# Performance work log

Hardware: AMD Instinct MI355X
Metric: run time of the kernel (lower is better)

## Reference

```python
import jax, jax.numpy as jnp
import numpy as np

FIELD = 32
DIM = 64
LAYER_SIZE = (128, 128)


def setup_inputs() -> dict:
    key = jax.random.key(0)
    ks = jax.random.split(key, 5)
    B = 4096
    x = jax.random.normal(ks[0], (B, FIELD, DIM), dtype=jnp.float32)
    # conv1d kernel-size-1 weights, stored as [out_channels, in_channels]
    field_nums = [FIELD]
    params = {}
    for i, size in enumerate(LAYER_SIZE):
        in_ch = field_nums[-1] * field_nums[0]
        fan = 1.0 / np.sqrt(in_ch)
        params[f"w{i}"] = jax.random.uniform(ks[1 + 2 * i % 4], (size, in_ch), minval=-fan, maxval=fan, dtype=jnp.float32)
        params[f"b{i}"] = jax.random.uniform(ks[2 + 2 * i % 4], (size,), minval=-fan, maxval=fan, dtype=jnp.float32)
        field_nums.append(size // 2)
    return {"cin_inputs": x, "w0": params["w0"], "b0": params["b0"], "w1": params["w1"], "b1": params["b1"]}


def _cin(x, weights, biases):
    # x: [B, F, D]
    B, F, D = x.shape
    hidden = x
    finals = []
    n_layers = len(weights)
    for i, (w, b) in enumerate(zip(weights, biases)):
        size = w.shape[0]
        # outer product over field dims: [B, H, F, D] -> reshape to [B, H*F, D]
        z = jnp.einsum('bhd,bfd->bhfd', hidden, x).reshape(B, hidden.shape[1] * F, D)
        # 1x1 conv over channel dim == per-position matmul
        y = jnp.einsum('bcd,oc->bod', z, w) + b[None, :, None]
        y = jax.nn.relu(y)
        if i != n_layers - 1:
            hidden, direct = y[:, : size // 2, :], y[:, size // 2 :, :]
        else:
            direct = y
        finals.append(direct)
    return jnp.concatenate(finals, axis=1).sum(-1)  # [B, out_dim]


def reference(cin_inputs, w0, b0, w1, b1):
    return _cin(cin_inputs, [w0, w1], [b0, b1])
```

## Files before the change

### kernel.cpp

```cpp
#include <hip/hip_runtime.h>
#include <hip/hip_fp16.h>


typedef __attribute__((ext_vector_type(8))) _Float16 f16x8;
typedef __attribute__((ext_vector_type(4))) float f32x4;
typedef __attribute__((ext_vector_type(4))) unsigned short us4;
typedef unsigned short ushortT;

__global__ void cin_pack_w(const float* __restrict__ w0,
                           const float* __restrict__ w1,
                           ushortT* __restrict__ wp) {
    int gidx = blockIdx.x * 256 + threadIdx.x;
    if (gidx >= 49152) return;
    const float* src;
    ushortT* dst;
    if (gidx < 16384) {
        int kk = gidx >> 9, rem = gidx & 511;
        int n = rem >> 6, lp = rem & 63;
        int o = n * 16 + (lp & 15);
        int c = kk * 32 + ((lp >> 4) << 3);
        src = w0 + o * 1024 + c;
        dst = wp + gidx * 8;
    } else {
        int g1 = gidx - 16384;
        int kk = g1 >> 9, rem = g1 & 511;
        int n = rem >> 6, lp = rem & 63;
        int o = n * 16 + (lp & 15);
        int c = kk * 32 + ((lp >> 4) << 3);
        src = w1 + o * 2048 + c;
        dst = wp + 131072 + g1 * 8;
    }
    ushortT tmp[8];
#pragma unroll
    for (int j = 0; j < 8; ++j) {
        __half h = __float2half(src[j]);
        tmp[j] = __builtin_bit_cast(ushortT, h);
    }
    *reinterpret_cast<f16x8*>(dst) = *reinterpret_cast<const f16x8*>(tmp);
}

__global__ __launch_bounds__(256, 2) void cin_mfma_kernel(
    const float* __restrict__ x,
    const float* __restrict__ b0,
    const float* __restrict__ b1,
    const ushortT* __restrict__ wp,
    float* __restrict__ out)
{
    const int tid = threadIdx.x;
    const int l   = tid & 63;
    const int w   = tid >> 6;
    const int b   = blockIdx.x * 4 + w;
    const int r16 = l & 15;
    const int g   = l >> 4;

    __shared__ ushortT Xh[4][2048];
    __shared__ ushortT Hsm[4][64 * 66];
    __shared__ __align__(16) ushortT Wb[2][4096];

    ushortT* Xw = Xh[w];
    ushortT* Hw = Hsm[w];

    const float* xb = x + (size_t)b * 2048;
#pragma unroll
    for (int i = 0; i < 8; ++i) {
        float4 v = reinterpret_cast<const float4*>(xb)[i * 64 + l];
        int flat = (i * 64 + l) * 4;
        us4 h;
        h[0] = __builtin_bit_cast(ushortT, __float2half(v.x));
        h[1] = __builtin_bit_cast(ushortT, __float2half(v.y));
        h[2] = __builtin_bit_cast(ushortT, __float2half(v.z));
        h[3] = __builtin_bit_cast(ushortT, __float2half(v.w));
        *reinterpret_cast<us4*>(&Xw[flat]) = h;
    }

#pragma unroll
    for (int c = 0; c < 2; ++c) {
        const char* src = (const char*)wp + (size_t)c * 8192 +
                          (size_t)(w * 2) * 1024 + (size_t)l * 16;
        __builtin_amdgcn_global_load_lds((const unsigned int*)src,
                                         (unsigned int*)&Wb[c][(w * 2) * 512], 16, 0, 0);
        __builtin_amdgcn_global_load_lds((const unsigned int*)(src + 1024),
                                         (unsigned int*)&Wb[c][(w * 2 + 1) * 512], 16, 0, 0);
    }
    __syncthreads();

    __half2 tf16[4][4];
#pragma unroll
    for (int mt = 0; mt < 4; ++mt)
#pragma unroll
        for (int p = 0; p < 4; ++p) {
            unsigned lo = Xw[(g * 8 + 2 * p) * 64 + mt * 16 + r16];
            unsigned hi = Xw[(g * 8 + 2 * p + 1) * 64 + mt * 16 + r16];
            tf16[mt][p] = __builtin_bit_cast(__half2, lo | (hi << 16));
        }

    __half2 th[4];
#pragma unroll
    for (int mt = 0; mt < 4; ++mt) {
        unsigned u = Xw[mt * 16 + r16];
        th[mt] = __builtin_bit_cast(__half2, (u << 16) | u);
    }
    f16x8 Bf[8];
#pragma unroll
    for (int n = 0; n < 8; ++n)
        Bf[n] = *reinterpret_cast<const f16x8*>(&Wb[0][n * 512 + l * 8]);

    __syncthreads();

    f32x4 acc[4][8];
#pragma unroll
    for (int mt = 0; mt < 4; ++mt)
#pragma unroll
        for (int n = 0; n < 8; ++n) acc[mt][n] = (f32x4){0.f, 0.f, 0.f, 0.f};

#pragma unroll 1
    for (int k = 0; k < 96; ++k) {
        const int cur = k & 1;

        if (k + 2 < 96) {
            const char* src = (const char*)wp + (size_t)(k + 2) * 8192 +
                              (size_t)(w * 2) * 1024 + (size_t)l * 16;
            __builtin_amdgcn_global_load_lds((const unsigned int*)src,
                (unsigned int*)&Wb[cur][(w * 2) * 512], 16, 0, 0);
            __builtin_amdgcn_global_load_lds((const unsigned int*)(src + 1024),
                (unsigned int*)&Wb[cur][(w * 2 + 1) * 512], 16, 0, 0);
        }

        const bool pf_th = (k < 95) && (k != 31);
        const ushortT* WbN = Wb[(k < 95) ? (cur ^ 1) : cur];
        const ushortT* thp = (k + 1 < 32) ? (Xw + (k + 1) * 64)
                                          : (Hw + (k - 31) * 66);

        union AfU { __half2 h2[4]; f16x8 v; };
        AfU Af[4];
#pragma unroll
        for (int mt = 0; mt < 4; ++mt)
#pragma unroll
            for (int p = 0; p < 4; ++p)
                Af[mt].h2[p] = __hmul2(tf16[mt][p], th[mt]);

        if (pf_th) {
#pragma unroll
            for (int mt = 0; mt < 4; ++mt) {
                unsigned u = thp[mt * 16 + r16];
                th[mt] = __builtin_bit_cast(__half2, (u << 16) | u);
            }
        }

#pragma unroll
        for (int n = 0; n < 8; ++n) {
#pragma unroll
            for (int mt = 0; mt < 4; ++mt)
                acc[mt][n] = __builtin_amdgcn_mfma_f32_16x16x32_f16(
                    Af[mt].v, Bf[n], acc[mt][n], 0, 0, 0);
            Bf[n] = *reinterpret_cast<const f16x8*>(&WbN[n * 512 + l * 8]);
        }

        __syncthreads();

        if (k == 31) {
#pragma unroll
            for (int n = 0; n < 4; ++n) {
                float bn = b0[n * 16 + r16];
#pragma unroll
                for (int mt = 0; mt < 4; ++mt)
#pragma unroll
                    for (int r = 0; r < 4; ++r) {
                        float y = fmaxf(acc[mt][n][r] + bn, 0.f);
                        int d = mt * 16 + g * 4 + r;
                        int o = n * 16 + r16;
                        __half hy = __float2half(y);
                        Hw[o * 66 + d] = __builtin_bit_cast(ushortT, hy);
                    }
            }
#pragma unroll
            for (int n = 4; n < 8; ++n) {
                float bn = b0[n * 16 + r16];
                float s = 0.f;
#pragma unroll
                for (int mt = 0; mt < 4; ++mt)
#pragma unroll
                    for (int r = 0; r < 4; ++r)
                        s += fmaxf(acc[mt][n][r] + bn, 0.f);
                s += __shfl_xor(s, 16);
                s += __shfl_xor(s, 32);
                if (l < 16) out[(size_t)b * 192 + (n - 4) * 16 + l] = s;
            }
#pragma unroll
            for (int mt = 0; mt < 4; ++mt)
#pragma unroll
                for (int n = 0; n < 8; ++n) acc[mt][n] = (f32x4){0.f, 0.f, 0.f, 0.f};
#pragma unroll
            for (int mt = 0; mt < 4; ++mt) {
                unsigned u = Hw[mt * 16 + r16];
                th[mt] = __builtin_bit_cast(__half2, (u << 16) | u);
            }
        }
    }

#pragma unroll
    for (int n = 0; n < 8; ++n) {
        float bn = b1[n * 16 + r16];
        float s = 0.f;
#pragma unroll
        for (int mt = 0; mt < 4; ++mt)
#pragma unroll
            for (int r = 0; r < 4; ++r)
                s += fmaxf(acc[mt][n][r] + bn, 0.f);
        s += __shfl_xor(s, 16);
        s += __shfl_xor(s, 32);
        if (l < 16) out[(size_t)b * 192 + 64 + n * 16 + l] = s;
    }
}

__global__ __launch_bounds__(256, 4) void cin_fp32_kernel(
    const float* __restrict__ x, const float* __restrict__ w0,
    const float* __restrict__ b0, const float* __restrict__ w1,
    const float* __restrict__ b1, float* __restrict__ out)
{
    const int b = blockIdx.x;
    const int tid = threadIdx.x;
    const int d = tid & 63;
    const int wave = tid >> 6;

    __shared__ float Xs[32][64];
    __shared__ float Hsf[64][64];

    const float* xb = x + (size_t)b * 2048;
    float treg[32];
#pragma unroll
    for (int f = 0; f < 32; ++f) treg[f] = xb[f * 64 + d];
    if (wave == 0) {
#pragma unroll
        for (int f = 0; f < 32; ++f) Xs[f][d] = treg[f];
    }
    __syncthreads();
    const int o_base = __builtin_amdgcn_readfirstlane(wave * 32);

    for (int oi = 0; oi < 32; ++oi) {
        const int o = o_base + oi;
        const float* wrow = w0 + (size_t)o * 1024;
        float acc = b0[o];
        for (int h = 0; h < 32; ++h) {
            const float* wv = wrow + h * 32;
            const float th = Xs[h][d];
            float s0 = 0.f, s1 = 0.f, s2 = 0.f, s3 = 0.f;
#pragma unroll
            for (int f = 0; f < 32; f += 4) {
                s0 = fmaf(wv[f + 0], treg[f + 0], s0);
                s1 = fmaf(wv[f + 1], treg[f + 1], s1);
                s2 = fmaf(wv[f + 2], treg[f + 2], s2);
                s3 = fmaf(wv[f + 3], treg[f + 3], s3);
            }
            acc = fmaf((s0 + s1) + (s2 + s3), th, acc);
        }
        float y = fmaxf(acc, 0.f);
        if (o < 64) {
            Hsf[o][d] = y;
        } else {
#pragma unroll
            for (int off = 32; off > 0; off >>= 1) y += __shfl_xor(y, off, 64);
            if (d == 0) out[(size_t)b * 192 + (o - 64)] = y;
        }
    }
    __syncthreads();

    for (int oi = 0; oi < 32; ++oi) {
        const int o = o_base + oi;
        const float* wrow = w1 + (size_t)o * 2048;
        float acc = b1[o];
        for (int h = 0; h < 64; ++h) {
            const float* wv = wrow + h * 32;
            const float th = Hsf[h][d];
            float s0 = 0.f, s1 = 0.f, s2 = 0.f, s3 = 0.f;
#pragma unroll
            for (int f = 0; f < 32; f += 4) {
                s0 = fmaf(wv[f + 0], treg[f + 0], s0);
                s1 = fmaf(wv[f + 1], treg[f + 1], s1);
                s2 = fmaf(wv[f + 2], treg[f + 2], s2);
                s3 = fmaf(wv[f + 3], treg[f + 3], s3);
            }
            acc = fmaf((s0 + s1) + (s2 + s3), th, acc);
        }
        float y = fmaxf(acc, 0.f);
#pragma unroll
        for (int off = 32; off > 0; off >>= 1) y += __shfl_xor(y, off, 64);
        if (d == 0) out[(size_t)b * 192 + 64 + o] = y;
    }
}

extern "C" void kernel_launch(void* const* d_in, const int* in_sizes, int n_in,
                              void* d_out, int out_size, void* d_ws, size_t ws_size,
                              hipStream_t stream) {
    const float* x  = (const float*)d_in[0];
    const float* w0 = (const float*)d_in[1];
    const float* b0 = (const float*)d_in[2];
    const float* w1 = (const float*)d_in[3];
    const float* b1 = (const float*)d_in[4];
    float* out = (float*)d_out;

    if (ws_size >= 786432) {
        ushortT* wp = (ushortT*)d_ws;
        cin_pack_w<<<192, 256, 0, stream>>>(w0, w1, wp);
        cin_mfma_kernel<<<1024, 256, 0, stream>>>(x, b0, b1, wp, out);
    } else {
        cin_fp32_kernel<<<4096, 256, 0, stream>>>(x, w0, b0, w1, b1, out);
    }
}
```

Before: 169.1 us.

## Process two K-steps per iteration with larger double-buffered weight tiles

The K loop is restructured so each iteration handles two 32-channel steps. It streams a 16 KB weight chunk per stage into a double buffer, which halves the number of block barriers and async-load issue points. The hidden-layer tile now reuses the per-wave X region, unpadded, and is written with vectorized stores, so shared memory shrinks slightly. MFMA bursts are wrapped in s_setprio to favour matrix issue. In exchange, th values are reloaded from LDS each step, and register pressure rises from holding two sets of B fragments.

```diff
diff --git a/kernel.cpp b/kernel.cpp
--- a/kernel.cpp
+++ b/kernel.cpp
@@ -53,12 +53,10 @@
     const int r16 = l & 15;
     const int g   = l >> 4;
 
-    __shared__ ushortT Xh[4][2048];
-    __shared__ ushortT Hsm[4][64 * 66];
-    __shared__ __align__(16) ushortT Wb[2][4096];
-
-    ushortT* Xw = Xh[w];
-    ushortT* Hw = Hsm[w];
+    __shared__ ushortT U[4][4096];
+    __shared__ __align__(16) ushortT Wb[2][8192];
+
+    ushortT* Xw = U[w];
 
     const float* xb = x + (size_t)b * 2048;
 #pragma unroll
@@ -74,13 +72,11 @@
     }
 
 #pragma unroll
-    for (int c = 0; c < 2; ++c) {
-        const char* src = (const char*)wp + (size_t)c * 8192 +
-                          (size_t)(w * 2) * 1024 + (size_t)l * 16;
+    for (int j = 0; j < 4; ++j) {
+        const int seg = w * 4 + j;
+        const char* src = (const char*)wp + (size_t)seg * 1024 + (size_t)l * 16;
         __builtin_amdgcn_global_load_lds((const unsigned int*)src,
-                                         (unsigned int*)&Wb[c][(w * 2) * 512], 16, 0, 0);
-        __builtin_amdgcn_global_load_lds((const unsigned int*)(src + 1024),
-                                         (unsigned int*)&Wb[c][(w * 2 + 1) * 512], 16, 0, 0);
+                                         (unsigned int*)&Wb[0][seg * 512], 16, 0, 0);
     }
     __syncthreads();
 
@@ -94,84 +90,102 @@
             tf16[mt][p] = __builtin_bit_cast(__half2, lo | (hi << 16));
         }
 
-    __half2 th[4];
-#pragma unroll
-    for (int mt = 0; mt < 4; ++mt) {
-        unsigned u = Xw[mt * 16 + r16];
-        th[mt] = __builtin_bit_cast(__half2, (u << 16) | u);
-    }
-    f16x8 Bf[8];
-#pragma unroll
-    for (int n = 0; n < 8; ++n)
-        Bf[n] = *reinterpret_cast<const f16x8*>(&Wb[0][n * 512 + l * 8]);
-
-    __syncthreads();
-
     f32x4 acc[4][8];
 #pragma unroll
     for (int mt = 0; mt < 4; ++mt)
 #pragma unroll
         for (int n = 0; n < 8; ++n) acc[mt][n] = (f32x4){0.f, 0.f, 0.f, 0.f};
 
+    union AfU { __half2 h2[4]; f16x8 v; };
+
 #pragma unroll 1
-    for (int k = 0; k < 96; ++k) {
-        const int cur = k & 1;
-
-        if (k + 2 < 96) {
-            const char* src = (const char*)wp + (size_t)(k + 2) * 8192 +
-                              (size_t)(w * 2) * 1024 + (size_t)l * 16;
-            __builtin_amdgcn_global_load_lds((const unsigned int*)src,
-                (unsigned int*)&Wb[cur][(w * 2) * 512], 16, 0, 0);
-            __builtin_amdgcn_global_load_lds((const unsigned int*)(src + 1024),
-                (unsigned int*)&Wb[cur][(w * 2 + 1) * 512], 16, 0, 0);
-        }
-
-        const bool pf_th = (k < 95) && (k != 31);
-        const ushortT* WbN = Wb[(k < 95) ? (cur ^ 1) : cur];
-        const ushortT* thp = (k + 1 < 32) ? (Xw + (k + 1) * 64)
-                                          : (Hw + (k - 31) * 66);
-
-        union AfU { __half2 h2[4]; f16x8 v; };
+    for (int p = 0; p < 48; ++p) {
+        const int ps = p & 1;
+        const int k0 = 2 * p;
+
+        if (p + 1 < 48) {
+#pragma unroll
+            for (int j = 0; j < 4; ++j) {
+                const int seg = w * 4 + j;
+                const char* src = (const char*)wp + (size_t)(p + 1) * 16384 +
+                                  (size_t)seg * 1024 + (size_t)l * 16;
+                __builtin_amdgcn_global_load_lds((const unsigned int*)src,
+                    (unsigned int*)&Wb[ps ^ 1][seg * 512], 16, 0, 0);
+            }
+        }
+
+        const ushortT* th0p = Xw + (size_t)((k0 < 32) ? k0 : (k0 - 32)) * 64;
+        __half2 th[4];
+#pragma unroll
+        for (int mt = 0; mt < 4; ++mt) {
+            unsigned u = th0p[mt * 16 + r16];
+            th[mt] = __builtin_bit_cast(__half2, (u << 16) | u);
+        }
+
+        f16x8 Bf[8];
+#pragma unroll
+        for (int n = 0; n < 8; ++n)
+            Bf[n] = *reinterpret_cast<const f16x8*>(&Wb[ps][n * 512 + l * 8]);
+
         AfU Af[4];
 #pragma unroll
         for (int mt = 0; mt < 4; ++mt)
 #pragma unroll
-            for (int p = 0; p < 4; ++p)
-                Af[mt].h2[p] = __hmul2(tf16[mt][p], th[mt]);
-
-        if (pf_th) {
-#pragma unroll
-            for (int mt = 0; mt < 4; ++mt) {
-                unsigned u = thp[mt * 16 + r16];
-                th[mt] = __builtin_bit_cast(__half2, (u << 16) | u);
-            }
-        }
-
+            for (int q = 0; q < 4; ++q)
+                Af[mt].h2[q] = __hmul2(tf16[mt][q], th[mt]);
+
+        const int k1 = k0 + 1;
+        const ushortT* th1p = Xw + (size_t)((k1 < 32) ? k1 : (k1 - 32)) * 64;
+#pragma unroll
+        for (int mt = 0; mt < 4; ++mt) {
+            unsigned u = th1p[mt * 16 + r16];
+            th[mt] = __builtin_bit_cast(__half2, (u << 16) | u);
+        }
+
+        __builtin_amdgcn_s_setprio(1);
 #pragma unroll
         for (int n = 0; n < 8; ++n) {
 #pragma unroll
             for (int mt = 0; mt < 4; ++mt)
                 acc[mt][n] = __builtin_amdgcn_mfma_f32_16x16x32_f16(
                     Af[mt].v, Bf[n], acc[mt][n], 0, 0, 0);
-            Bf[n] = *reinterpret_cast<const f16x8*>(&WbN[n * 512 + l * 8]);
-        }
+            Bf[n] = *reinterpret_cast<const f16x8*>(&Wb[ps][4096 + n * 512 + l * 8]);
+        }
+        __builtin_amdgcn_s_setprio(0);
+
+#pragma unroll
+        for (int mt = 0; mt < 4; ++mt)
+#pragma unroll
+            for (int q = 0; q < 4; ++q)
+                Af[mt].h2[q] = __hmul2(tf16[mt][q], th[mt]);
+
+        __builtin_amdgcn_s_setprio(1);
+#pragma unroll
+        for (int n = 0; n < 8; ++n)
+#pragma unroll
+            for (int mt = 0; mt < 4; ++mt)
+                acc[mt][n] = __builtin_amdgcn_mfma_f32_16x16x32_f16(
+                    Af[mt].v, Bf[n], acc[mt][n], 0, 0, 0);
+        __builtin_amdgcn_s_setprio(0);
 
         __syncthreads();
 
-        if (k == 31) {
+        if (p == 15) {
+            ushortT* Hw = Xw;
 #pragma unroll
             for (int n = 0; n < 4; ++n) {
                 float bn = b0[n * 16 + r16];
 #pragma unroll
-                for (int mt = 0; mt < 4; ++mt)
+                for (int mt = 0; mt < 4; ++mt) {
+                    us4 hv;
 #pragma unroll
                     for (int r = 0; r < 4; ++r) {
                         float y = fmaxf(acc[mt][n][r] + bn, 0.f);
-                        int d = mt * 16 + g * 4 + r;
-                        int o = n * 16 + r16;
-                        __half hy = __float2half(y);
-                        Hw[o * 66 + d] = __builtin_bit_cast(ushortT, hy);
+                        hv[r] = __builtin_bit_cast(ushortT, __float2half(y));
                     }
+                    const int o = n * 16 + r16;
+                    *reinterpret_cast<us4*>(&Hw[o * 64 + mt * 16 + g * 4]) = hv;
+                }
             }
 #pragma unroll
             for (int n = 4; n < 8; ++n) {
@@ -190,11 +204,6 @@
             for (int mt = 0; mt < 4; ++mt)
 #pragma unroll
                 for (int n = 0; n < 8; ++n) acc[mt][n] = (f32x4){0.f, 0.f, 0.f, 0.f};
-#pragma unroll
-            for (int mt = 0; mt < 4; ++mt) {
-                unsigned u = Hw[mt * 16 + r16];
-                th[mt] = __builtin_bit_cast(__half2, (u << 16) | u);
-            }
         }
     }
 
```

New measurement: 162.5 us. 1.04x faster.
